# Kernel tuning notes

Measured on AMD Instinct MI355X. Metric: run time of the kernel, lower is better.

The kernel has to match this reference:

```python
import jax, jax.numpy as jnp
import numpy as np

NUM_HEADS = 8
CHUNK = 64


def setup_inputs() -> dict:
    key = jax.random.key(0)
    k1, k2, k3, k4 = jax.random.split(key, 4)
    B, C, H, W = 16, 384, 64, 64
    x = jax.random.normal(k1, (B, C, H, W), dtype=jnp.float32)
    # torch nn.Linear weights are [out, in]; qkv has no bias (qkv_bias=False)
    qkv_w = jax.random.normal(k2, (3 * C, C), dtype=jnp.float32) * (C ** -0.5)
    proj_w = jax.random.normal(k3, (C, C), dtype=jnp.float32) * (C ** -0.5)
    proj_b = jax.random.normal(k4, (C,), dtype=jnp.float32) * 0.02
    return {"x": x, "qkv_w": qkv_w, "proj_w": proj_w, "proj_b": proj_b}


def reference(x, qkv_w, proj_w, proj_b):
    B, C, H, W = x.shape
    N = H * W
    nh = NUM_HEADS
    hd = C // nh
    scale = hd ** -0.5
    nc = N // CHUNK  # number of non-overlapping local blocks

    t = x.reshape(B, C, N).transpose(0, 2, 1)  # [B, N, C]
    qkv = t @ qkv_w.T  # [B, N, 3C]
    qkv = qkv.reshape(B, N, 3, nh, hd).transpose(2, 0, 3, 1, 4)  # [3, B, nh, N, hd]
    q, k, v = qkv[0], qkv[1], qkv[2]

    # block-local attention: reshape N -> (nc, CHUNK) and batch over blocks
    q = q.reshape(B, nh, nc, CHUNK, hd)
    k = k.reshape(B, nh, nc, CHUNK, hd)
    v = v.reshape(B, nh, nc, CHUNK, hd)

    scores = jnp.einsum('bhnqd,bhnkd->bhnqk', q, k) * scale  # [B,nh,nc,CHUNK,CHUNK]
    attn = jax.nn.softmax(scores, axis=-1)
    out = jnp.einsum('bhnqk,bhnkd->bhnqd', attn, v)  # [B,nh,nc,CHUNK,hd]

    out = out.reshape(B, nh, N, hd).transpose(0, 2, 1, 3).reshape(B, N, C)
    out = out @ proj_w.T + proj_b
    return out.transpose(0, 2, 1).reshape(B, C, H, W)
```

## Files before the change

### kernel.cpp

```cpp
#include <hip/hip_runtime.h>
#include <stdint.h>

#define NH 8
#define HD 48
#define CC 384
#define NN 4096
#define CK 384

typedef short short8 __attribute__((ext_vector_type(8)));
typedef float floatx4 __attribute__((ext_vector_type(4)));

__device__ inline unsigned short f32_to_bf16_bits(float f) {
    uint32_t u = __builtin_bit_cast(uint32_t, f);
    u = (u + 0x7FFFu + ((u >> 16) & 1u)) >> 16;
    return (unsigned short)u;
}
__device__ inline short8 load8(const unsigned short* p) {
    return *reinterpret_cast<const short8*>(p);
}
typedef __attribute__((address_space(1))) const void gvoid_t;
typedef __attribute__((address_space(3))) void lvoid_t;
__device__ inline void async16(const unsigned short* g, unsigned short* l) {
    __builtin_amdgcn_global_load_lds((gvoid_t*)g, (lvoid_t*)l, 16, 0, 0);
}

__global__ __launch_bounds__(256) void k_cvt(
    const float* __restrict__ src, unsigned short* __restrict__ dst, int n8)
{
    int i = blockIdx.x * 256 + threadIdx.x;
    if (i >= n8) return;
    const float* s = src + (size_t)i * 8;
    unsigned short t[8];
    #pragma unroll
    for (int j = 0; j < 8; ++j) t[j] = f32_to_bf16_bits(s[j]);
    *reinterpret_cast<short8*>(dst + (size_t)i * 8) = *reinterpret_cast<short8*>(t);
}

__global__ __launch_bounds__(256) void k_tr(
    const float* __restrict__ x, unsigned short* __restrict__ xT)
{
    __shared__ unsigned short tile[64][72];
    int bx = blockIdx.x;
    int nt = bx & 63; int rest = bx >> 6; int ct = rest % 6; int b = rest / 6;
    int c0 = ct * 64, n0 = nt * 64;
    int t = threadIdx.x;
    int nl = t & 63, w = t >> 6;
    const float* xb = x + (size_t)b * CC * NN;
    #pragma unroll
    for (int i = 0; i < 4; ++i) {
        int cl = w * 16 + i * 4;
        unsigned short u[4];
        #pragma unroll
        for (int j = 0; j < 4; ++j)
            u[j] = f32_to_bf16_bits(xb[(size_t)(c0 + cl + j) * NN + n0 + nl]);
        *reinterpret_cast<uint2*>(&tile[nl][cl]) = *reinterpret_cast<uint2*>(u);
    }
    __syncthreads();
    #pragma unroll
    for (int it = 0; it < 2; ++it) {
        int v = it * 256 + t;
        int row = v >> 3, seg = v & 7;
        *reinterpret_cast<short8*>(xT + ((size_t)b * NN + n0 + row) * CK + c0 + seg * 8) =
            load8(&tile[row][seg * 8]);
    }
}

__global__ __launch_bounds__(256) void k_qkv(
    const unsigned short* __restrict__ A,
    const unsigned short* __restrict__ W,
    unsigned short* __restrict__ QK,
    unsigned short* __restrict__ Vt)
{
    __shared__ unsigned short smem[17408];
    unsigned short* As = smem;
    unsigned short* Ws = smem + 8192;
    int bx = blockIdx.x;
    int l  = (bx & 7) * 576 + (bx >> 3);
    int tf = l % 9, tm = l / 9;
    int m0 = tm * 128, f0 = tf * 128;
    int tid = threadIdx.x, wid = tid >> 6, lane = tid & 63;
    int l15 = lane & 15, quad = lane >> 4;
    int wm = wid & 1, wn = wid >> 1;

    const unsigned short* Ab = A + (size_t)m0 * CK;
    const unsigned short* Wb = W + (size_t)f0 * CK;

    floatx4 acc[4][4] = {};

    for (int kk = 0; kk < 6; ++kk) {
        int k0 = kk * 64;
        #pragma unroll
        for (int i = 0; i < 4; ++i) {
            int c = i * 256 + tid;
            async16(Ab + (size_t)(c >> 3) * CK + k0 + (c & 7) * 8, As + (i * 256 + wid * 64) * 8);
            async16(Wb + (size_t)(c >> 3) * CK + k0 + (c & 7) * 8, Ws + (i * 256 + wid * 64) * 8);
        }
        __syncthreads();
        #pragma unroll
        for (int ks = 0; ks < 2; ++ks) {
            short8 a[4], bf[4];
            #pragma unroll
            for (int i = 0; i < 4; ++i)
                a[i] = load8(As + (wm * 64 + i * 16 + l15) * 64 + ks * 32 + quad * 8);
            #pragma unroll
            for (int j = 0; j < 4; ++j)
                bf[j] = load8(Ws + (wn * 64 + j * 16 + l15) * 64 + ks * 32 + quad * 8);
            #pragma unroll
            for (int i = 0; i < 4; ++i)
                #pragma unroll
                for (int j = 0; j < 4; ++j)
                    acc[i][j] = __builtin_amdgcn_mfma_f32_16x16x32_bf16(a[i], bf[j], acc[i][j], 0, 0, 0);
        }
        __syncthreads();
    }

    int b = m0 >> 12, nb = m0 & 4095;
    if (tf < 6) {
        #pragma unroll
        for (int i = 0; i < 4; ++i)
            #pragma unroll
            for (int j = 0; j < 4; ++j)
                #pragma unroll
                for (int r = 0; r < 4; ++r)
                    smem[(wm * 64 + i * 16 + quad * 4 + r) * 128 + wn * 64 + j * 16 + l15] =
                        f32_to_bf16_bits(acc[i][j][r]);
        __syncthreads();
        #pragma unroll
        for (int it = 0; it < 8; ++it) {
            int c = it * 256 + tid;
            int row = c >> 4, seg = c & 15;
            *reinterpret_cast<short8*>(QK + (size_t)(m0 + row) * 768 + f0 + seg * 8) =
                load8(smem + row * 128 + seg * 8);
        }
    } else {
        #pragma unroll
        for (int i = 0; i < 4; ++i)
            #pragma unroll
            for (int j = 0; j < 4; ++j)
                #pragma unroll
                for (int r = 0; r < 4; ++r)
                    smem[(wn * 64 + j * 16 + l15) * 136 + wm * 64 + i * 16 + quad * 4 + r] =
                        f32_to_bf16_bits(acc[i][j][r]);
        __syncthreads();
        int fvb = (tf - 6) * 128;
        #pragma unroll
        for (int it = 0; it < 8; ++it) {
            int c = it * 256 + tid;
            int fl = c >> 4, seg = c & 15;
            int fv = fvb + fl;
            int h = fv / 48, d = fv - h * 48;
            *reinterpret_cast<short8*>(Vt + (((size_t)(b * 8 + h) * 48 + d) << 12) + nb + seg * 8) =
                load8(smem + fl * 136 + seg * 8);
        }
    }
}

__global__ __launch_bounds__(256) void k_attn(
    const unsigned short* __restrict__ QK,
    const unsigned short* __restrict__ Vt,
    unsigned short* __restrict__ AO)
{
    __shared__ unsigned short ql[64][64];
    __shared__ unsigned short kl[64][64];
    __shared__ unsigned short vt[48][72];
    __shared__ float          sc[64][66];
    __shared__ unsigned short pl[64][72];

    int bx = blockIdx.x;
    int cn = bx & 63, h = (bx >> 6) & 7, b = bx >> 9;
    int n0 = cn * 64;
    int tid = threadIdx.x, wid = tid >> 6, lane = tid & 63;
    int l15 = lane & 15, quad = lane >> 4;
    int m0w = wid * 16;
    int h48 = h * 48;
    size_t b4 = (size_t)b * NN + n0;

    for (int v = tid; v < 768; v += 256) {
        int mat = v / 384;
        int idx = v - mat * 384;
        int rr = idx / 6, seg = idx - rr * 6;
        uint4 val = *reinterpret_cast<const uint4*>(QK + (b4 + rr) * 768 + mat * 384 + h48 + seg * 8);
        unsigned short* dst = mat ? &kl[rr][seg * 8] : &ql[rr][seg * 8];
        *reinterpret_cast<uint4*>(dst) = val;
    }
    {
        short8 z = {};
        int v = tid;
        if (v < 256) {
            int mat = v >> 7, rr = (v >> 1) & 63, half = v & 1;
            unsigned short* dst = mat ? &kl[rr][48 + half * 8] : &ql[rr][48 + half * 8];
            *reinterpret_cast<short8*>(dst) = z;
        }
    }
    for (int v = tid; v < 384; v += 256) {
        int d = v >> 3, seg = v & 7;
        *reinterpret_cast<uint4*>(&vt[d][seg * 8]) =
            *reinterpret_cast<const uint4*>(Vt + (((size_t)(b * 8 + h) * 48 + d) << 12) + n0 + seg * 8);
    }
    __syncthreads();

    const float scale = 0.14433756729740643f;
    #pragma unroll
    for (int t = 0; t < 4; ++t) {
        floatx4 sacc = {};
        #pragma unroll
        for (int ks = 0; ks < 2; ++ks) {
            short8 a  = load8(&ql[m0w + l15][ks * 32 + quad * 8]);
            short8 bb = load8(&kl[t * 16 + l15][ks * 32 + quad * 8]);
            sacc = __builtin_amdgcn_mfma_f32_16x16x32_bf16(a, bb, sacc, 0, 0, 0);
        }
        #pragma unroll
        for (int r = 0; r < 4; ++r)
            sc[m0w + quad * 4 + r][t * 16 + l15] = sacc[r] * scale;
    }
    __syncthreads();

    {
        int row = m0w + l15;
        int jb  = quad * 16;
        float ev[16];
        #pragma unroll
        for (int jj = 0; jj < 16; ++jj) ev[jj] = sc[row][jb + jj];
        float m = ev[0];
        #pragma unroll
        for (int jj = 1; jj < 16; ++jj) m = fmaxf(m, ev[jj]);
        m = fmaxf(m, __shfl_xor(m, 16));
        m = fmaxf(m, __shfl_xor(m, 32));
        float s = 0.f;
        #pragma unroll
        for (int jj = 0; jj < 16; ++jj) { ev[jj] = __expf(ev[jj] - m); s += ev[jj]; }
        s += __shfl_xor(s, 16);
        s += __shfl_xor(s, 32);
        float inv = 1.0f / s;
        #pragma unroll
        for (int jj = 0; jj < 16; ++jj) pl[row][jb + jj] = f32_to_bf16_bits(ev[jj] * inv);
    }
    __syncthreads();

    #pragma unroll
    for (int t = 0; t < 3; ++t) {
        floatx4 oacc = {};
        #pragma unroll
        for (int ks = 0; ks < 2; ++ks) {
            short8 a  = load8(&pl[m0w + l15][ks * 32 + quad * 8]);
            short8 bb = load8(&vt[t * 16 + l15][ks * 32 + quad * 8]);
            oacc = __builtin_amdgcn_mfma_f32_16x16x32_bf16(a, bb, oacc, 0, 0, 0);
        }
        #pragma unroll
        for (int r = 0; r < 4; ++r)
            kl[m0w + quad * 4 + r][t * 16 + l15] = f32_to_bf16_bits(oacc[r]);
    }
    __syncthreads();

    for (int v = tid; v < 384; v += 256) {
        int rr = v / 6, seg = v - rr * 6;
        *reinterpret_cast<short8*>(AO + (b4 + rr) * CC + h48 + seg * 8) =
            load8(&kl[rr][seg * 8]);
    }
}

__global__ __launch_bounds__(256) void k_proj(
    const unsigned short* __restrict__ A,
    const unsigned short* __restrict__ W,
    const float* __restrict__ bias,
    float* __restrict__ out)
{
    __shared__ unsigned short smem[17408];
    unsigned short* As = smem;
    unsigned short* Ws = smem + 8192;
    float* fs = (float*)smem;
    int bx = blockIdx.x;
    int l  = (bx & 7) * 192 + (bx >> 3);
    int tf = l % 3, tm = l / 3;
    int m0 = tm * 128, f0 = tf * 128;
    int tid = threadIdx.x, wid = tid >> 6, lane = tid & 63;
    int l15 = lane & 15, quad = lane >> 4;
    int wm = wid & 1, wn = wid >> 1;

    const unsigned short* Ab = A + (size_t)m0 * CK;
    const unsigned short* Wb = W + (size_t)f0 * CK;

    floatx4 acc[4][4] = {};

    for (int kk = 0; kk < 6; ++kk) {
        int k0 = kk * 64;
        #pragma unroll
        for (int i = 0; i < 4; ++i) {
            int c = i * 256 + tid;
            async16(Ab + (size_t)(c >> 3) * CK + k0 + (c & 7) * 8, As + (i * 256 + wid * 64) * 8);
            async16(Wb + (size_t)(c >> 3) * CK + k0 + (c & 7) * 8, Ws + (i * 256 + wid * 64) * 8);
        }
        __syncthreads();
        #pragma unroll
        for (int ks = 0; ks < 2; ++ks) {
            short8 a[4], bf[4];
            #pragma unroll
            for (int i = 0; i < 4; ++i)
                a[i] = load8(As + (wm * 64 + i * 16 + l15) * 64 + ks * 32 + quad * 8);
            #pragma unroll
            for (int j = 0; j < 4; ++j)
                bf[j] = load8(Ws + (wn * 64 + j * 16 + l15) * 64 + ks * 32 + quad * 8);
            #pragma unroll
            for (int i = 0; i < 4; ++i)
                #pragma unroll
                for (int j = 0; j < 4; ++j)
                    acc[i][j] = __builtin_amdgcn_mfma_f32_16x16x32_bf16(a[i], bf[j], acc[i][j], 0, 0, 0);
        }
        __syncthreads();
    }

    int b = m0 >> 12, nb = m0 & 4095;
    #pragma unroll
    for (int hh = 0; hh < 2; ++hh) {
        if (wn == hh) {
            #pragma unroll
            for (int j = 0; j < 4; ++j) {
                float bv = bias[f0 + hh * 64 + j * 16 + l15];
                #pragma unroll
                for (int i = 0; i < 4; ++i)
                    #pragma unroll
                    for (int r = 0; r < 4; ++r)
                        fs[(j * 16 + l15) * 132 + wm * 64 + i * 16 + quad * 4 + r] =
                            acc[i][j][r] + bv;
            }
        }
        __syncthreads();
        #pragma unroll
        for (int it = 0; it < 8; ++it) {
            int c = it * 256 + tid;
            int cl = c >> 5, seg = c & 31;
            *reinterpret_cast<float4*>(
                out + (((size_t)(b * CC + f0 + hh * 64 + cl)) << 12) + nb + seg * 4) =
                *reinterpret_cast<const float4*>(fs + cl * 132 + seg * 4);
        }
        __syncthreads();
    }
}

extern "C" void kernel_launch(void* const* d_in, const int* in_sizes, int n_in,
                              void* d_out, int out_size, void* d_ws, size_t ws_size,
                              hipStream_t stream) {
    const float* x      = (const float*)d_in[0];
    const float* qkv_w  = (const float*)d_in[1];
    const float* proj_w = (const float*)d_in[2];
    const float* proj_b = (const float*)d_in[3];
    float* out = (float*)d_out;

    const size_t nX  = (size_t)16 * CC * NN;
    const size_t nW1 = (size_t)3 * CC * CC;
    const size_t nW2 = (size_t)CC * CC;

    unsigned short* xT  = (unsigned short*)d_ws;
    unsigned short* w1b = xT  + nX;
    unsigned short* w2b = w1b + nW1;
    unsigned short* QK  = w2b + nW2;
    unsigned short* Vt  = QK  + (size_t)16 * NN * 768;
    unsigned short* AO  = Vt  + (size_t)16 * 8 * 48 * NN;

    k_tr  <<<dim3(16 * 6 * 64), dim3(256), 0, stream>>>(x, xT);
    k_cvt <<<dim3((int)(nW1 / 8 + 255) / 256), dim3(256), 0, stream>>>(qkv_w, w1b, (int)(nW1 / 8));
    k_cvt <<<dim3((int)(nW2 / 8 + 255) / 256), dim3(256), 0, stream>>>(proj_w, w2b, (int)(nW2 / 8));

    k_qkv <<<dim3(512 * 9), dim3(256), 0, stream>>>(xT, w1b, QK, Vt);
    k_attn<<<dim3(16 * 8 * 64), dim3(256), 0, stream>>>(QK, Vt, AO);
    k_proj<<<dim3(512 * 3), dim3(256), 0, stream>>>(AO, w2b, proj_b, out);
}
```

Measured before the change: 377.4 us.

## Double-buffer LDS tiles in QKV and projection GEMMs to overlap loads with MFMA

Result: faster. 353.7 us (-6.3%).

```diff
diff --git a/kernel.cpp b/kernel.cpp
--- a/kernel.cpp
+++ b/kernel.cpp
@@ -71,9 +71,7 @@
     unsigned short* __restrict__ QK,
     unsigned short* __restrict__ Vt)
 {
-    __shared__ unsigned short smem[17408];
-    unsigned short* As = smem;
-    unsigned short* Ws = smem + 8192;
+    __shared__ unsigned short smem[32768];
     int bx = blockIdx.x;
     int l  = (bx & 7) * 576 + (bx >> 3);
     int tf = l % 9, tm = l / 9;
@@ -87,15 +85,27 @@
 
     floatx4 acc[4][4] = {};
 
-    for (int kk = 0; kk < 6; ++kk) {
-        int k0 = kk * 64;
+    auto stage = [&](int kt, int buf) {
+        int k0 = kt * 64;
+        unsigned short* Asd = smem + buf * 16384;
+        unsigned short* Wsd = Asd + 8192;
         #pragma unroll
         for (int i = 0; i < 4; ++i) {
             int c = i * 256 + tid;
-            async16(Ab + (size_t)(c >> 3) * CK + k0 + (c & 7) * 8, As + (i * 256 + wid * 64) * 8);
-            async16(Wb + (size_t)(c >> 3) * CK + k0 + (c & 7) * 8, Ws + (i * 256 + wid * 64) * 8);
-        }
-        __syncthreads();
+            async16(Ab + (size_t)(c >> 3) * CK + k0 + (c & 7) * 8, Asd + (i * 256 + wid * 64) * 8);
+            async16(Wb + (size_t)(c >> 3) * CK + k0 + (c & 7) * 8, Wsd + (i * 256 + wid * 64) * 8);
+        }
+    };
+
+    stage(0, 0);
+    __syncthreads();
+
+    int cur = 0;
+    #pragma unroll
+    for (int kk = 0; kk < 6; ++kk) {
+        if (kk < 5) stage(kk + 1, cur ^ 1);
+        unsigned short* As = smem + cur * 16384;
+        unsigned short* Ws = As + 8192;
         #pragma unroll
         for (int ks = 0; ks < 2; ++ks) {
             short8 a[4], bf[4];
@@ -112,6 +122,7 @@
                     acc[i][j] = __builtin_amdgcn_mfma_f32_16x16x32_bf16(a[i], bf[j], acc[i][j], 0, 0, 0);
         }
         __syncthreads();
+        cur ^= 1;
     }
 
     int b = m0 >> 12, nb = m0 & 4095;
@@ -265,9 +276,7 @@
     const float* __restrict__ bias,
     float* __restrict__ out)
 {
-    __shared__ unsigned short smem[17408];
-    unsigned short* As = smem;
-    unsigned short* Ws = smem + 8192;
+    __shared__ unsigned short smem[32768];
     float* fs = (float*)smem;
     int bx = blockIdx.x;
     int l  = (bx & 7) * 192 + (bx >> 3);
@@ -282,15 +291,27 @@
 
     floatx4 acc[4][4] = {};
 
-    for (int kk = 0; kk < 6; ++kk) {
-        int k0 = kk * 64;
+    auto stage = [&](int kt, int buf) {
+        int k0 = kt * 64;
+        unsigned short* Asd = smem + buf * 16384;
+        unsigned short* Wsd = Asd + 8192;
         #pragma unroll
         for (int i = 0; i < 4; ++i) {
             int c = i * 256 + tid;
-            async16(Ab + (size_t)(c >> 3) * CK + k0 + (c & 7) * 8, As + (i * 256 + wid * 64) * 8);
-            async16(Wb + (size_t)(c >> 3) * CK + k0 + (c & 7) * 8, Ws + (i * 256 + wid * 64) * 8);
-        }
-        __syncthreads();
+            async16(Ab + (size_t)(c >> 3) * CK + k0 + (c & 7) * 8, Asd + (i * 256 + wid * 64) * 8);
+            async16(Wb + (size_t)(c >> 3) * CK + k0 + (c & 7) * 8, Wsd + (i * 256 + wid * 64) * 8);
+        }
+    };
+
+    stage(0, 0);
+    __syncthreads();
+
+    int cur = 0;
+    #pragma unroll
+    for (int kk = 0; kk < 6; ++kk) {
+        if (kk < 5) stage(kk + 1, cur ^ 1);
+        unsigned short* As = smem + cur * 16384;
+        unsigned short* Ws = As + 8192;
         #pragma unroll
         for (int ks = 0; ks < 2; ++ks) {
             short8 a[4], bf[4];
@@ -307,6 +328,7 @@
                     acc[i][j] = __builtin_amdgcn_mfma_f32_16x16x32_bf16(a[i], bf[j], acc[i][j], 0, 0, 0);
         }
         __syncthreads();
+        cur ^= 1;
     }
 
     int b = m0 >> 12, nb = m0 & 4095;
```
